# Performance work log

Hardware: AMD Instinct MI355X
Metric: run time of the kernel (lower is better)

Reference implementation:

```python
import jax, jax.numpy as jnp
import numpy as np

M0, M1, H = 128, 64, 8            # scalar mul, vector mul, num heads
AH0, AH1 = 16, 8                  # per-head irreps: 16x0e + 8x1e
D = M0 + 3 * M1                   # 320 node feature dim
DTP0 = M0 + M1                    # 192 scalar channels out of depthwise TP
DTP1 = M0 + 2 * M1                # 256 vector channels out of depthwise TP
WNUM = 2 * M0 + 3 * M1            # 448 TP path weights (uvu, edge mul=1)
RAD_IN, RAD_HID = 32, 64
N_NODES, N_EDGES = 10000, 160000
INV_SQRT3 = 1.0 / np.sqrt(3.0)    # CG norm for 1e x 1e -> 0e
INV_SQRT2 = 1.0 / np.sqrt(2.0)    # CG norm for 1e x 1e -> 1e


def _split(x, m0, m1):
    # e3nn layout: [m0 scalars | m1 vectors * 3 components]
    return x[..., :m0], x[..., m0:].reshape(x.shape[:-1] + (m1, 3))


def _silu(x):
    return x * jax.nn.sigmoid(x)


def _smooth_leaky(x, a=0.2):
    # SmoothLeakyReLU from equiformer
    return 0.5 * (1 + a) * x + 0.5 * (1 - a) * x * (2.0 * jax.nn.sigmoid(x) - 1.0)


def _dtp(s, v, e0, e1, w):
    # depthwise (uvu) tensor product of (M0x0e + M1x1e) with edge attr (1x0e + 1x1e)
    # s [E,M0], v [E,M1,3], e0 [E,1], e1 [E,3], w [E,WNUM] or [WNUM] (internal)
    w1, w2, w3, w4, w5 = jnp.split(w, [M0, 2 * M0, 2 * M0 + M1, 2 * M0 + 2 * M1], axis=-1)
    os1 = w1 * s * e0                                                  # 0e x 0e -> 0e
    os2 = w4 * (jnp.einsum('emc,ec->em', v, e1) * INV_SQRT3)           # 1e x 1e -> 0e
    ov1 = (w2 * s)[..., None] * e1[:, None, :]                         # 0e x 1e -> 1e
    ov2 = w3[..., None] * v * e0[..., None]                            # 1e x 0e -> 1e
    ov3 = w5[..., None] * (jnp.cross(v, e1[:, None, :]) * INV_SQRT2)   # 1e x 1e -> 1e
    return jnp.concatenate([os1, os2], -1), jnp.concatenate([ov1, ov2, ov3], -2)


def _forward(node_input, edge_src, edge_dst, edge_attr, edge_scalars,
             Wsrc_s, Wsrc_v, bsrc, Wdst_s, Wdst_v,
             rad_W1, rad_b1, rad_W2, rad_off,
             Wact_s, bact, Wact_v, Walpha, balpha, w_int,
             Wval_s, bval, Wval_v, alpha_dot, Wproj_s, bproj, Wproj_v):
    N = node_input.shape[0]
    E = edge_src.shape[0]
    s, v = _split(node_input, M0, M1)
    # merge_src / merge_dst: per-irrep linear (bias only on scalars of src)
    ms_s = s @ Wsrc_s + bsrc
    ms_v = jnp.einsum('nmc,mk->nkc', v, Wsrc_v)
    md_s = s @ Wdst_s
    md_v = jnp.einsum('nmc,mk->nkc', v, Wdst_v)
    msg_s = ms_s[edge_src] + md_s[edge_dst]          # [E, M0]
    msg_v = ms_v[edge_src] + md_v[edge_dst]          # [E, M1, 3]
    e0, e1 = edge_attr[:, :1], edge_attr[:, 1:4]
    # radial profile MLP -> edge-dependent TP weights
    w = _silu(edge_scalars @ rad_W1 + rad_b1) @ rad_W2 + rad_off       # [E, WNUM]
    ds, dv = _dtp(msg_s, msg_v, e0, e1, w)           # [E, DTP0], [E, DTP1, 3]
    # alpha branch: linear on TP scalars -> heads -> smooth leaky -> dot
    al = _smooth_leaky((ds @ Walpha + balpha).reshape(E, H, AH0))
    logits = jnp.einsum('ehk,hk->eh', al, alpha_dot[0])                # [E, H]
    # value branch: sep_act.lin + gate
    scal = ds @ Wact_s + bact                        # [E, M0+M1] scalars+gates
    gated_v = jnp.einsum('emc,mk->ekc', dv, Wact_v)  # [E, M1, 3]
    val_s = _silu(scal[:, :M0])
    val_v = gated_v * jax.nn.sigmoid(scal[:, M0:])[..., None]
    # sep_value: depthwise TP with internal weights + linear
    vs, vv = _dtp(val_s, val_v, e0, e1, w_int)
    out_s = vs @ Wval_s + bval                       # [E, H*AH0]
    out_v = jnp.einsum('emc,mk->ekc', vv, Wval_v)    # [E, H*AH1, 3]
    value = jnp.concatenate([out_s.reshape(E, H, AH0),
                             out_v.reshape(E, H, AH1 * 3)], axis=2)    # [E, H, 40]
    # softmax over incoming edges per destination node
    mx = jax.lax.stop_gradient(jax.ops.segment_max(logits, edge_dst, num_segments=N))
    mx = jnp.where(jnp.isfinite(mx), mx, 0.0)
    ex = jnp.exp(logits - mx[edge_dst])
    den = jax.ops.segment_sum(ex, edge_dst, num_segments=N)
    alpha = ex / (den[edge_dst] + 1e-16)             # [E, H]
    agg = jax.ops.segment_sum(value * alpha[..., None], edge_dst, num_segments=N)
    # heads2vec + output projection
    node_s = agg[:, :, :AH0].reshape(N, H * AH0)
    node_v = agg[:, :, AH0:].reshape(N, H * AH1, 3)
    po_s = node_s @ Wproj_s + bproj
    po_v = jnp.einsum('nmc,mk->nkc', node_v, Wproj_v)
    return jnp.concatenate([po_s, po_v.reshape(N, M1 * 3)], axis=1)


def _lin(key, fi, fo):
    return jax.random.normal(key, (fi, fo), jnp.float32) / np.sqrt(fi)


def setup_inputs() -> dict:
    ks = iter(jax.random.split(jax.random.key(0), 40))
    inp = {}
    inp['node_input'] = jax.random.normal(next(ks), (N_NODES, D), jnp.float32)
    inp['edge_src'] = jax.random.randint(next(ks), (N_EDGES,), 0, N_NODES)
    inp['edge_dst'] = jax.random.randint(next(ks), (N_EDGES,), 0, N_NODES)
    inp['edge_attr'] = jax.random.normal(next(ks), (N_EDGES, 4), jnp.float32)
    inp['edge_scalars'] = jax.random.normal(next(ks), (N_EDGES, RAD_IN), jnp.float32)
    inp['Wsrc_s'] = _lin(next(ks), M0, M0)
    inp['Wsrc_v'] = _lin(next(ks), M1, M1)
    inp['bsrc'] = 0.1 * jax.random.normal(next(ks), (M0,), jnp.float32)
    inp['Wdst_s'] = _lin(next(ks), M0, M0)
    inp['Wdst_v'] = _lin(next(ks), M1, M1)
    inp['rad_W1'] = _lin(next(ks), RAD_IN, RAD_HID)
    inp['rad_b1'] = 0.1 * jax.random.normal(next(ks), (RAD_HID,), jnp.float32)
    inp['rad_W2'] = _lin(next(ks), RAD_HID, WNUM)
    inp['rad_off'] = 0.1 * jax.random.normal(next(ks), (WNUM,), jnp.float32)
    inp['Wact_s'] = _lin(next(ks), DTP0, M0 + M1)
    inp['bact'] = 0.1 * jax.random.normal(next(ks), (M0 + M1,), jnp.float32)
    inp['Wact_v'] = _lin(next(ks), DTP1, M1)
    inp['Walpha'] = _lin(next(ks), DTP0, H * AH0)
    inp['balpha'] = 0.1 * jax.random.normal(next(ks), (H * AH0,), jnp.float32)
    inp['w_int'] = jax.random.normal(next(ks), (WNUM,), jnp.float32)
    inp['Wval_s'] = _lin(next(ks), DTP0, H * AH0)
    inp['bval'] = 0.1 * jax.random.normal(next(ks), (H * AH0,), jnp.float32)
    inp['Wval_v'] = _lin(next(ks), DTP1, H * AH1)
    inp['alpha_dot'] = jax.random.normal(next(ks), (1, H, AH0), jnp.float32) / np.sqrt(AH0)
    inp['Wproj_s'] = _lin(next(ks), H * AH0, M0)
    inp['bproj'] = 0.1 * jax.random.normal(next(ks), (M0,), jnp.float32)
    inp['Wproj_v'] = _lin(next(ks), H * AH1, M1)
    return inp


def reference(node_input, edge_src, edge_dst, edge_attr, edge_scalars,
              Wsrc_s, Wsrc_v, bsrc, Wdst_s, Wdst_v,
              rad_W1, rad_b1, rad_W2, rad_off,
              Wact_s, bact, Wact_v, Walpha, balpha, w_int,
              Wval_s, bval, Wval_v, alpha_dot, Wproj_s, bproj, Wproj_v):
    return _forward(node_input, edge_src, edge_dst, edge_attr, edge_scalars,
                    Wsrc_s, Wsrc_v, bsrc, Wdst_s, Wdst_v,
                    rad_W1, rad_b1, rad_W2, rad_off,
                    Wact_s, bact, Wact_v, Walpha, balpha, w_int,
                    Wval_s, bval, Wval_v, alpha_dot, Wproj_s, bproj, Wproj_v)
```

## Files before the change

kernel.cpp:

```cpp
#include <hip/hip_runtime.h>

#define NN 10000
#define NE 160000
#define INV_SQRT3f 0.57735026918962576f
#define INV_SQRT2f 0.70710678118654752f
#define VPL 640000

typedef short bshort8 __attribute__((ext_vector_type(8)));
typedef float floatx4 __attribute__((ext_vector_type(4)));
#define MFMA16(a,b,c) __builtin_amdgcn_mfma_f32_16x16x32_bf16((a),(b),(c),0,0,0)

__device__ __forceinline__ float sigm(float x){ return 1.f/(1.f+__expf(-x)); }
__device__ __forceinline__ float siluf(float x){ return x*sigm(x); }
__device__ __forceinline__ float sleaky(float x){ return 0.6f*x + 0.4f*x*(2.f*sigm(x)-1.f); }
__device__ __forceinline__ unsigned short f2bf(float f){
  return (unsigned short)((__float_as_uint(f) + 0x8000u)>>16);
}
__device__ __forceinline__ float bf2f(unsigned short h){
  return __uint_as_float(((unsigned)h)<<16);
}

#define O_W1   0
#define O_W2   2048
#define O_WAS  30720
#define O_WAVT 67584
#define O_WAVB 75776
#define O_WVS  83968
#define O_WVVT 108544
#define O_WVVB 116736
#define O_WALP 124928
#define SWZ_TOTAL 149504

__global__ __launch_bounds__(256) void k_init(float* __restrict__ num,
                                              float* __restrict__ den,
                                              int* __restrict__ cnt) {
  int i = blockIdx.x*256 + threadIdx.x;
  if (i < NN*320) num[i] = 0.f;
  if (i < NN*8) den[i] = 0.f;
  if (i < NN) cnt[i] = 0;
}

__global__ __launch_bounds__(256) void k_hist(const int* __restrict__ edst,
                                              int* __restrict__ cnt) {
  int e = blockIdx.x*256 + threadIdx.x;
  if (e < NE) atomicAdd(&cnt[edst[e]], 1);
}

__global__ __launch_bounds__(256) void k_scan(const int* __restrict__ cnt,
                                              int* __restrict__ offs) {
  __shared__ int wsum[4];
  const int tid = threadIdx.x;
  const int lane = tid & 63, wave = tid >> 6;
  int v[40]; int s = 0;
  #pragma unroll
  for (int j=0;j<40;j++){ int i = tid*40+j; v[j] = (i<NN)?cnt[i]:0; s += v[j]; }
  int incl = s;
  #pragma unroll
  for (int d=1; d<64; d<<=1) { int t = __shfl_up(incl, d, 64); if (lane>=d) incl += t; }
  if (lane==63) wsum[wave] = incl;
  __syncthreads();
  int wbase = 0;
  for (int w=0; w<wave; ++w) wbase += wsum[w];
  int excl = wbase + incl - s;
  #pragma unroll
  for (int j=0;j<40;j++){ int i = tid*40+j; if (i<NN) offs[i] = excl; excl += v[j]; }
}

__global__ __launch_bounds__(256) void k_scatter(const int* __restrict__ edst,
                                                 int* __restrict__ offs,
                                                 int* __restrict__ perm) {
  int e = blockIdx.x*256 + threadIdx.x;
  if (e < NE) {
    int pos = atomicAdd(&offs[edst[e]], 1);
    perm[pos] = e;
  }
}

__global__ __launch_bounds__(256) void node_pre(
    const float* __restrict__ x,
    const float* __restrict__ Wsrc_s, const float* __restrict__ Wsrc_v,
    const float* __restrict__ bsrc,
    const float* __restrict__ Wdst_s, const float* __restrict__ Wdst_v,
    float* __restrict__ ms_s, float* __restrict__ md_s,
    float* __restrict__ ms_v, float* __restrict__ md_v) {
  __shared__ __align__(16) float s_s[128*8];
  __shared__ __align__(16) float s_v[192*8];
  const int tid = threadIdx.x;
  const int n0 = blockIdx.x*8;
  for (int idx = tid; idx < 8*320; idx += 256) {
    int n = idx/320, d = idx - n*320;
    float val = x[(n0+n)*320 + d];
    if (d < 128) s_s[d*8+n] = val;
    else         s_v[(d-128)*8+n] = val;
  }
  __syncthreads();
  {
    int g = tid>>7, j = tid&127;
    float accs[4], accd[4];
    float b = bsrc[j];
    #pragma unroll
    for (int i=0;i<4;i++){ accs[i]=b; accd[i]=0.f; }
    for (int k=0;k<128;k++) {
      float w1 = Wsrc_s[k*128+j], w2 = Wdst_s[k*128+j];
      float4 sv = *(const float4*)&s_s[k*8+g*4];
      accs[0]+=sv.x*w1; accs[1]+=sv.y*w1; accs[2]+=sv.z*w1; accs[3]+=sv.w*w1;
      accd[0]+=sv.x*w2; accd[1]+=sv.y*w2; accd[2]+=sv.z*w2; accd[3]+=sv.w*w2;
    }
    #pragma unroll
    for (int i=0;i<4;i++){ int n=n0+g*4+i; ms_s[n*128+j]=accs[i]; md_s[n*128+j]=accd[i]; }
  }
  if (tid < 192) {
    int c = tid>>6, k = tid&63;
    float accs[8], accd[8];
    #pragma unroll
    for (int e=0;e<8;e++){ accs[e]=0.f; accd[e]=0.f; }
    for (int m=0;m<64;m++) {
      float w1 = Wsrc_v[m*64+k], w2 = Wdst_v[m*64+k];
      float4 v0 = *(const float4*)&s_v[(m*3+c)*8];
      float4 v1 = *(const float4*)&s_v[(m*3+c)*8+4];
      accs[0]+=v0.x*w1; accs[1]+=v0.y*w1; accs[2]+=v0.z*w1; accs[3]+=v0.w*w1;
      accs[4]+=v1.x*w1; accs[5]+=v1.y*w1; accs[6]+=v1.z*w1; accs[7]+=v1.w*w1;
      accd[0]+=v0.x*w2; accd[1]+=v0.y*w2; accd[2]+=v0.z*w2; accd[3]+=v0.w*w2;
      accd[4]+=v1.x*w2; accd[5]+=v1.y*w2; accd[6]+=v1.z*w2; accd[7]+=v1.w*w2;
    }
    #pragma unroll
    for (int e=0;e<8;e++){
      int n=n0+e;
      ms_v[c*VPL + n*64 + k] = accs[e];
      md_v[c*VPL + n*64 + k] = accd[e];
    }
  }
}

__global__ __launch_bounds__(256) void k_prep(
    const float* __restrict__ W1, const float* __restrict__ W2,
    const float* __restrict__ WAs, const float* __restrict__ WAv,
    const float* __restrict__ WVs, const float* __restrict__ WVv,
    const float* __restrict__ WAl,
    unsigned short* __restrict__ swz) {
  int s = blockIdx.x*256 + threadIdx.x;
  if (s >= SWZ_TOTAL) return;
  const float* src; int base, N, KT, rowOff;
  if      (s < 2048)  { base=O_W1;   src=W1;  N=64;  KT=1; rowOff=0; }
  else if (s < 30720) { base=O_W2;   src=W2;  N=448; KT=2; rowOff=0; }
  else if (s < 67584) { base=O_WAS;  src=WAs; N=192; KT=6; rowOff=0; }
  else if (s < 75776) { base=O_WAVT; src=WAv; N=64;  KT=4; rowOff=0; }
  else if (s < 83968) { base=O_WAVB; src=WAv; N=64;  KT=4; rowOff=128; }
  else if (s < 108544){ base=O_WVS;  src=WVs; N=128; KT=6; rowOff=0; }
  else if (s < 116736){ base=O_WVVT; src=WVv; N=64;  KT=4; rowOff=0; }
  else if (s < 124928){ base=O_WVVB; src=WVv; N=64;  KT=4; rowOff=128; }
  else                { base=O_WALP; src=WAl; N=128; KT=6; rowOff=0; }
  int loc = s - base;
  int j = loc & 7, l = (loc>>3)&63, kt = (loc>>9)%KT, nt = loc/(512*KT);
  int row = kt*32 + (l>>4)*8 + j + rowOff;
  int col = nt*16 + (l&15);
  swz[s] = f2bf(src[row*N + col]);
}

__global__ __launch_bounds__(256, 4) void e_all(
    const float* __restrict__ ms_s, const float* __restrict__ md_s,
    const float* __restrict__ ms_v, const float* __restrict__ md_v,
    const int* __restrict__ esrc, const int* __restrict__ edst,
    const int* __restrict__ perm,
    const float* __restrict__ eattr, const float* __restrict__ escal,
    const float* __restrict__ rad_b1, const float* __restrict__ rad_off,
    const float* __restrict__ bact, const float* __restrict__ w_int,
    const float* __restrict__ bval,
    const float* __restrict__ balpha, const float* __restrict__ alpha_dot,
    const unsigned short* __restrict__ swz,
    float* __restrict__ den, float* __restrict__ num) {
  __shared__ __align__(16) char smem[39040];
  unsigned short* sw   = (unsigned short*)smem;
  float* vout          = (float*)smem;
  unsigned short* ads  = (unsigned short*)(smem+14336);
  unsigned short* at1  = (unsigned short*)(smem+20736);
  unsigned short* advb = (unsigned short*)(smem+25088);
  unsigned short* aes  = (unsigned short*)(smem+25088);
  unsigned short* ah   = (unsigned short*)(smem+26368);
  float* s_e0 = (float*)(smem+38144);
  float* s_e1 = (float*)(smem+38208);
  float* s_ex = (float*)(smem+38400);
  int* s_src  = (int*)(smem+38912);
  int* s_dst  = (int*)(smem+38976);
  int* s_eid  = (int*)(smem+38848);
  const int tid  = threadIdx.x;
  const int lane = tid & 63, wave = tid >> 6;
  const int quad = lane >> 4, l15 = lane & 15;
  const int eb = blockIdx.x*16;

  if (tid < 16) {
    int eid = perm[eb+tid];
    s_eid[tid] = eid; s_src[tid] = esrc[eid]; s_dst[tid] = edst[eid];
  }
  __syncthreads();
  if (tid >= 64 && tid < 128) {
    int t = tid-64, e = t>>2, q = t&3;
    float a = eattr[s_eid[e]*4+q];
    if (q == 0) s_e0[e] = a; else s_e1[(q-1)*16+e] = a;
  }
  #pragma unroll
  for (int it = 0; it < 2; ++it) {
    int idx = tid + it*256;
    int e = idx>>5, i = idx&31;
    aes[e*40+i] = f2bf(escal[s_eid[e]*32+i]);
  }
  __syncthreads();

  {
    int nt = wave, col = nt*16 + l15;
    bshort8 a = *(const bshort8*)&aes[l15*40 + quad*8];
    bshort8 b = *(const bshort8*)&swz[O_W1 + (nt*64 + lane)*8];
    float bb = rad_b1[col];
    floatx4 acc = {bb,bb,bb,bb};
    acc = MFMA16(a, b, acc);
    #pragma unroll
    for (int r=0;r<4;r++) ah[(quad*4+r)*72 + col] = f2bf(siluf(acc[r]));
  }
  __syncthreads();

  {
    bshort8 ha0 = *(const bshort8*)&ah[l15*72 + quad*8];
    bshort8 ha1 = *(const bshort8*)&ah[l15*72 + 32 + quad*8];
    #pragma unroll
    for (int t=0;t<7;t++) {
      int nt = wave*7 + t, col = nt*16 + l15;
      float o = rad_off[col];
      floatx4 acc = {o,o,o,o};
      acc = MFMA16(ha0, *(const bshort8*)&swz[O_W2 + ((nt*2+0)*64+lane)*8], acc);
      acc = MFMA16(ha1, *(const bshort8*)&swz[O_W2 + ((nt*2+1)*64+lane)*8], acc);
      #pragma unroll
      for (int r=0;r<4;r++) sw[(quad*4+r)*448 + col] = f2bf(acc[r]);
    }
  }
  __syncthreads();

  #pragma unroll
  for (int it = 0; it < 8; ++it) {
    int t = tid + it*256;
    int m = t&127, e = t>>7;
    float msgs = ms_s[s_src[e]*128+m] + md_s[s_dst[e]*128+m];
    ads[e*200+m] = f2bf(bf2f(sw[e*448+m])*msgs*s_e0[e]);
    at1[e*136+m] = f2bf(bf2f(sw[e*448+128+m])*msgs);
  }
  #pragma unroll
  for (int it = 0; it < 4; ++it) {
    int t = tid + it*256;
    int k = t&63, e = t>>6;
    int sb = s_src[e]*64 + k, db = s_dst[e]*64 + k;
    float vx = ms_v[0*VPL+sb] + md_v[0*VPL+db];
    float vy = ms_v[1*VPL+sb] + md_v[1*VPL+db];
    float vz = ms_v[2*VPL+sb] + md_v[2*VPL+db];
    float ex1 = s_e1[0+e], ey1 = s_e1[16+e], ez1 = s_e1[32+e];
    float d = vx*ex1 + vy*ey1 + vz*ez1;
    ads[e*200+128+k] = f2bf(bf2f(sw[e*448+320+k])*d*INV_SQRT3f);
    float w3v = bf2f(sw[e*448+256+k])*s_e0[e];
    float w5  = bf2f(sw[e*448+384+k])*INV_SQRT2f;
    advb[0*2176 + e*136 + k] = f2bf(w3v*vx);
    advb[1*2176 + e*136 + k] = f2bf(w3v*vy);
    advb[2*2176 + e*136 + k] = f2bf(w3v*vz);
    advb[0*2176 + e*136 + 64+k] = f2bf(w5*(vy*ez1 - vz*ey1));
    advb[1*2176 + e*136 + 64+k] = f2bf(w5*(vz*ex1 - vx*ez1));
    advb[2*2176 + e*136 + 64+k] = f2bf(w5*(vx*ey1 - vy*ex1));
  }
  __syncthreads();

  floatx4 sc0, sc1, sc2, gsa, gb0, gb1, gb2;
  {
    bshort8 fa[6];
    #pragma unroll
    for (int kt=0;kt<6;kt++) fa[kt] = *(const bshort8*)&ads[l15*200 + kt*32 + quad*8];
    #pragma unroll
    for (int t=0;t<2;t++) {
      int h = wave*2 + t;
      int col = h*16 + l15;
      float bb = balpha[col];
      floatx4 acc = {bb,bb,bb,bb};
      #pragma unroll
      for (int kt=0;kt<6;kt++)
        acc = MFMA16(fa[kt], *(const bshort8*)&swz[O_WALP + ((h*6+kt)*64+lane)*8], acc);
      float ad = alpha_dot[col];
      #pragma unroll
      for (int r=0;r<4;r++) {
        float p = sleaky(acc[r])*ad;
        p += __shfl_xor(p, 1);
        p += __shfl_xor(p, 2);
        p += __shfl_xor(p, 4);
        p += __shfl_xor(p, 8);
        if (l15 == 0) {
          int row = quad*4 + r;
          float ex = __expf(p);
          s_ex[row*8+h] = ex;
          atomicAdd(&den[s_dst[row]*8+h], ex);
        }
      }
    }
    {
      float bb = bact[wave*16 + l15];
      floatx4 a0 = {bb,bb,bb,bb};
      #pragma unroll
      for (int kt=0;kt<6;kt++)
        a0 = MFMA16(fa[kt], *(const bshort8*)&swz[O_WAS + ((wave*6+kt)*64+lane)*8], a0);
      sc0 = a0;
    }
    {
      float bb = bact[(wave+4)*16 + l15];
      floatx4 a1 = {bb,bb,bb,bb};
      #pragma unroll
      for (int kt=0;kt<6;kt++)
        a1 = MFMA16(fa[kt], *(const bshort8*)&swz[O_WAS + (((wave+4)*6+kt)*64+lane)*8], a1);
      sc1 = a1;
    }
    {
      float bb = bact[(wave+8)*16 + l15];
      floatx4 a2 = {bb,bb,bb,bb};
      #pragma unroll
      for (int kt=0;kt<6;kt++)
        a2 = MFMA16(fa[kt], *(const bshort8*)&swz[O_WAS + (((wave+8)*6+kt)*64+lane)*8], a2);
      sc2 = a2;
    }
    bshort8 ft[4];
    #pragma unroll
    for (int kt=0;kt<4;kt++) ft[kt] = *(const bshort8*)&at1[l15*136 + kt*32 + quad*8];
    {
      floatx4 acc = {0.f,0.f,0.f,0.f};
      #pragma unroll
      for (int kt=0;kt<4;kt++)
        acc = MFMA16(ft[kt], *(const bshort8*)&swz[O_WAVT + ((wave*4+kt)*64+lane)*8], acc);
      gsa = acc;
    }
    #pragma unroll
    for (int c=0;c<3;c++) {
      floatx4 acc = {0.f,0.f,0.f,0.f};
      #pragma unroll
      for (int kt=0;kt<4;kt++) {
        bshort8 fb = *(const bshort8*)&advb[c*2176 + l15*136 + kt*32 + quad*8];
        acc = MFMA16(fb, *(const bshort8*)&swz[O_WAVB + ((wave*4+kt)*64+lane)*8], acc);
      }
      if (c==0) gb0 = acc; else if (c==1) gb1 = acc; else gb2 = acc;
    }
  }
  __syncthreads();

  {
    const int k = wave*16 + l15;
    #pragma unroll
    for (int r=0;r<4;r++) {
      int row = quad*4 + r;
      float e0 = s_e0[row];
      {
        float v = siluf(sc0[r]);
        ads[row*200+k] = f2bf(w_int[k]*v*e0);
        at1[row*136+k] = f2bf(w_int[128+k]*v);
      }
      {
        int m = 64+k;
        float v = siluf(sc1[r]);
        ads[row*200+m] = f2bf(w_int[m]*v*e0);
        at1[row*136+m] = f2bf(w_int[128+m]*v);
      }
      {
        float sg = sigm(sc2[r]);
        float gs = gsa[r];
        float ex1 = s_e1[0+row], ey1 = s_e1[16+row], ez1 = s_e1[32+row];
        float v0 = (gs*ex1 + gb0[r])*sg;
        float v1 = (gs*ey1 + gb1[r])*sg;
        float v2 = (gs*ez1 + gb2[r])*sg;
        float d = v0*ex1 + v1*ey1 + v2*ez1;
        ads[row*200+128+k] = f2bf(w_int[320+k]*d*INV_SQRT3f);
        float w3v = w_int[256+k]*e0;
        float w5  = w_int[384+k]*INV_SQRT2f;
        advb[0*2176 + row*136 + k] = f2bf(w3v*v0);
        advb[1*2176 + row*136 + k] = f2bf(w3v*v1);
        advb[2*2176 + row*136 + k] = f2bf(w3v*v2);
        advb[0*2176 + row*136 + 64+k] = f2bf(w5*(v1*ez1 - v2*ey1));
        advb[1*2176 + row*136 + 64+k] = f2bf(w5*(v2*ex1 - v0*ez1));
        advb[2*2176 + row*136 + 64+k] = f2bf(w5*(v0*ey1 - v1*ex1));
      }
    }
  }
  __syncthreads();

  {
    bshort8 fa[6];
    #pragma unroll
    for (int kt=0;kt<6;kt++) fa[kt] = *(const bshort8*)&ads[l15*200 + kt*32 + quad*8];
    #pragma unroll
    for (int t=0;t<2;t++) {
      int h = wave + 4*t;
      float bb = bval[h*16 + l15];
      floatx4 acc = {bb,bb,bb,bb};
      #pragma unroll
      for (int kt=0;kt<6;kt++)
        acc = MFMA16(fa[kt], *(const bshort8*)&swz[O_WVS + ((h*6+kt)*64+lane)*8], acc);
      #pragma unroll
      for (int r=0;r<4;r++) {
        int row = quad*4 + r;
        vout[row*128 + h*16 + l15] = acc[r]*s_ex[row*8+h];
      }
    }
  }
  __syncthreads();

  {
    int j = tid & 127, g = tid >> 7;
    int h = j>>4, jj = j&15;
    float acc = 0.f; int cur = s_dst[g*8];
    #pragma unroll
    for (int e = g*8; e < g*8+8; ++e) {
      int d = s_dst[e];
      if (d != cur) { atomicAdd(&num[cur*320 + h*40 + jj], acc); acc = 0.f; cur = d; }
      acc += vout[e*128 + j];
    }
    atomicAdd(&num[cur*320 + h*40 + jj], acc);
  }
  __syncthreads();

  {
    bshort8 ft[4];
    #pragma unroll
    for (int kt=0;kt<4;kt++) ft[kt] = *(const bshort8*)&at1[l15*136 + kt*32 + quad*8];
    floatx4 vsh = {0.f,0.f,0.f,0.f};
    #pragma unroll
    for (int kt=0;kt<4;kt++)
      vsh = MFMA16(ft[kt], *(const bshort8*)&swz[O_WVVT + ((wave*4+kt)*64+lane)*8], vsh);
    int k = wave*16 + l15;
    int h = k>>3, q = k&7;
    #pragma unroll
    for (int c=0;c<3;c++) {
      floatx4 acc = {0.f,0.f,0.f,0.f};
      #pragma unroll
      for (int kt=0;kt<4;kt++) {
        bshort8 fb = *(const bshort8*)&advb[c*2176 + l15*136 + kt*32 + quad*8];
        acc = MFMA16(fb, *(const bshort8*)&swz[O_WVVB + ((wave*4+kt)*64+lane)*8], acc);
      }
      #pragma unroll
      for (int r=0;r<4;r++) {
        int row = quad*4 + r;
        vout[row*192 + h*24 + q*3 + c] =
            (acc[r] + s_e1[c*16+row]*vsh[r]) * s_ex[row*8+h];
      }
    }
  }
  __syncthreads();

  #pragma unroll
  for (int it = 0; it < 2; ++it) {
    int idx = tid + it*256;
    if (idx < 384) {
      int g = idx/192, jj = idx - g*192;
      int h = jj/24, rr = jj - h*24;
      float acc = 0.f; int cur = s_dst[g*8];
      #pragma unroll
      for (int e = g*8; e < g*8+8; ++e) {
        int d = s_dst[e];
        if (d != cur) { atomicAdd(&num[cur*320 + h*40 + 16 + rr], acc); acc = 0.f; cur = d; }
        acc += vout[e*192 + jj];
      }
      atomicAdd(&num[cur*320 + h*40 + 16 + rr], acc);
    }
  }
}

__global__ __launch_bounds__(256) void node_post(
    const float* __restrict__ num, const float* __restrict__ den,
    const float* __restrict__ Wproj_s, const float* __restrict__ bproj,
    const float* __restrict__ Wproj_v, float* __restrict__ out) {
  __shared__ __align__(16) float s_ns[128*8];
  __shared__ __align__(16) float s_nv[192*8];
  const int tid = threadIdx.x;
  const int n0 = blockIdx.x*8;
  for (int idx = tid; idx < 8*320; idx += 256) {
    int n = idx/320, j = idx - n*320;
    int h = j/40, r = j - h*40;
    float a = num[(n0+n)*320+j] / (den[(n0+n)*8+h] + 1e-16f);
    if (r < 16) s_ns[(h*16+r)*8+n] = a;
    else        s_nv[(h*24 + (r-16))*8+n] = a;
  }
  __syncthreads();
  {
    int g = tid>>7, j = tid&127;
    float acc[4]; float b = bproj[j];
    #pragma unroll
    for (int i=0;i<4;i++) acc[i]=b;
    for (int k=0;k<128;k++) {
      float wv = Wproj_s[k*128+j];
      float4 s4 = *(const float4*)&s_ns[k*8+g*4];
      acc[0]+=s4.x*wv; acc[1]+=s4.y*wv; acc[2]+=s4.z*wv; acc[3]+=s4.w*wv;
    }
    #pragma unroll
    for (int i=0;i<4;i++) out[(n0+g*4+i)*320 + j] = acc[i];
  }
  if (tid < 192) {
    int c = tid>>6, k = tid&63;
    float acc[8];
    #pragma unroll
    for (int e=0;e<8;e++) acc[e]=0.f;
    for (int m=0;m<64;m++) {
      float wv = Wproj_v[m*64+k];
      float4 v0 = *(const float4*)&s_nv[(m*3+c)*8];
      float4 v1 = *(const float4*)&s_nv[(m*3+c)*8+4];
      acc[0]+=v0.x*wv; acc[1]+=v0.y*wv; acc[2]+=v0.z*wv; acc[3]+=v0.w*wv;
      acc[4]+=v1.x*wv; acc[5]+=v1.y*wv; acc[6]+=v1.z*wv; acc[7]+=v1.w*wv;
    }
    #pragma unroll
    for (int e=0;e<8;e++) out[(n0+e)*320 + 128 + k*3 + c] = acc[e];
  }
}

extern "C" void kernel_launch(void* const* d_in, const int* in_sizes, int n_in,
                              void* d_out, int out_size, void* d_ws, size_t ws_size,
                              hipStream_t stream) {
  (void)in_sizes; (void)n_in; (void)out_size; (void)ws_size;
  const float* node_input = (const float*)d_in[0];
  const int*   esrc       = (const int*)d_in[1];
  const int*   edst       = (const int*)d_in[2];
  const float* eattr      = (const float*)d_in[3];
  const float* escal      = (const float*)d_in[4];
  const float* Wsrc_s     = (const float*)d_in[5];
  const float* Wsrc_v     = (const float*)d_in[6];
  const float* bsrc       = (const float*)d_in[7];
  const float* Wdst_s     = (const float*)d_in[8];
  const float* Wdst_v     = (const float*)d_in[9];
  const float* rad_W1     = (const float*)d_in[10];
  const float* rad_b1     = (const float*)d_in[11];
  const float* rad_W2     = (const float*)d_in[12];
  const float* rad_off    = (const float*)d_in[13];
  const float* Wact_s     = (const float*)d_in[14];
  const float* bact       = (const float*)d_in[15];
  const float* Wact_v     = (const float*)d_in[16];
  const float* Walpha     = (const float*)d_in[17];
  const float* balpha     = (const float*)d_in[18];
  const float* w_int      = (const float*)d_in[19];
  const float* Wval_s     = (const float*)d_in[20];
  const float* bval       = (const float*)d_in[21];
  const float* Wval_v     = (const float*)d_in[22];
  const float* alpha_dot  = (const float*)d_in[23];
  const float* Wproj_s    = (const float*)d_in[24];
  const float* bproj      = (const float*)d_in[25];
  const float* Wproj_v    = (const float*)d_in[26];
  float* out = (float*)d_out;

  float* ws = (float*)d_ws;
  float* ms_s   = ws;
  float* md_s   = ws + 1280000;
  float* ms_v   = ws + 2560000;
  float* md_v   = ws + 4480000;
  float* den    = ws + 6400000;
  float* num    = ws + 6480000;
  unsigned short* swz = (unsigned short*)(ws + 9680000);
  int* cnt  = (int*)(ws + 9754752);
  int* offs = (int*)(ws + 9764752);
  int* perm = (int*)(ws + 9774752);

  k_prep<<<584, 256, 0, stream>>>(rad_W1, rad_W2, Wact_s, Wact_v, Wval_s, Wval_v, Walpha, swz);
  k_init<<<12500, 256, 0, stream>>>(num, den, cnt);
  k_hist<<<625, 256, 0, stream>>>(edst, cnt);
  k_scan<<<1, 256, 0, stream>>>(cnt, offs);
  k_scatter<<<625, 256, 0, stream>>>(edst, offs, perm);
  node_pre<<<1250, 256, 0, stream>>>(node_input, Wsrc_s, Wsrc_v, bsrc, Wdst_s, Wdst_v,
                                     ms_s, md_s, ms_v, md_v);
  e_all<<<10000, 256, 0, stream>>>(ms_s, md_s, ms_v, md_v, esrc, edst, perm, eattr, escal,
                                   rad_b1, rad_off, bact, w_int, bval,
                                   balpha, alpha_dot, swz, den, num);
  node_post<<<1250, 256, 0, stream>>>(num, den, Wproj_s, bproj, Wproj_v, out);
}
```

Before: 449.9 us.

## Keep radial scalar weights in registers and shrink shared memory for occupancy

The radial MLP output tiles for the scalar TP weights now stay in MFMA accumulators and are consumed directly, so only the vector-path weights (192 columns) go to shared memory. The scalar value-output reduction is done in registers with direct atomics instead of a shared-memory staging pass and barrier. The vector output staging is stored as bf16, and together these shrink LDS from about 39 KB to about 31 KB, with launch bounds raised to 5 blocks per CU. Storing the vector output in bf16 before accumulation adds rounding error, and register pressure rises under the tighter occupancy bound.

```diff
diff --git a/kernel.cpp b/kernel.cpp
--- a/kernel.cpp
+++ b/kernel.cpp
@@ -157,7 +157,7 @@
   swz[s] = f2bf(src[row*N + col]);
 }
 
-__global__ __launch_bounds__(256, 4) void e_all(
+__global__ __launch_bounds__(256, 5) void e_all(
     const float* __restrict__ ms_s, const float* __restrict__ md_s,
     const float* __restrict__ ms_v, const float* __restrict__ md_v,
     const int* __restrict__ esrc, const int* __restrict__ edst,
@@ -169,20 +169,20 @@
     const float* __restrict__ balpha, const float* __restrict__ alpha_dot,
     const unsigned short* __restrict__ swz,
     float* __restrict__ den, float* __restrict__ num) {
-  __shared__ __align__(16) char smem[39040];
-  unsigned short* sw   = (unsigned short*)smem;
-  float* vout          = (float*)smem;
-  unsigned short* ads  = (unsigned short*)(smem+14336);
-  unsigned short* at1  = (unsigned short*)(smem+20736);
-  unsigned short* advb = (unsigned short*)(smem+25088);
-  unsigned short* aes  = (unsigned short*)(smem+25088);
-  unsigned short* ah   = (unsigned short*)(smem+26368);
-  float* s_e0 = (float*)(smem+38144);
-  float* s_e1 = (float*)(smem+38208);
-  float* s_ex = (float*)(smem+38400);
-  int* s_src  = (int*)(smem+38912);
-  int* s_dst  = (int*)(smem+38976);
-  int* s_eid  = (int*)(smem+38848);
+  __shared__ __align__(16) char smem[30912];
+  unsigned short* swv   = (unsigned short*)smem;
+  unsigned short* voutv = (unsigned short*)smem;
+  unsigned short* ads  = (unsigned short*)(smem+6144);
+  unsigned short* at1  = (unsigned short*)(smem+12544);
+  unsigned short* advb = (unsigned short*)(smem+16896);
+  unsigned short* aes  = (unsigned short*)(smem+16896);
+  unsigned short* ah   = (unsigned short*)(smem+18176);
+  float* s_e0 = (float*)(smem+29952);
+  float* s_e1 = (float*)(smem+30016);
+  float* s_ex = (float*)(smem+30208);
+  int* s_eid  = (int*)(smem+30720);
+  int* s_src  = (int*)(smem+30784);
+  int* s_dst  = (int*)(smem+30848);
   const int tid  = threadIdx.x;
   const int lane = tid & 63, wave = tid >> 6;
   const int quad = lane >> 4, l15 = lane & 15;
@@ -218,30 +218,50 @@
   }
   __syncthreads();
 
+  floatx4 wA0, wA1, wB0, wB1;
   {
     bshort8 ha0 = *(const bshort8*)&ah[l15*72 + quad*8];
     bshort8 ha1 = *(const bshort8*)&ah[l15*72 + 32 + quad*8];
-    #pragma unroll
-    for (int t=0;t<7;t++) {
-      int nt = wave*7 + t, col = nt*16 + l15;
-      float o = rad_off[col];
+    { int nt = wave;       float o = rad_off[nt*16+l15]; floatx4 a = {o,o,o,o};
+      a = MFMA16(ha0, *(const bshort8*)&swz[O_W2 + ((nt*2+0)*64+lane)*8], a);
+      a = MFMA16(ha1, *(const bshort8*)&swz[O_W2 + ((nt*2+1)*64+lane)*8], a); wA0 = a; }
+    { int nt = 8+wave;     float o = rad_off[nt*16+l15]; floatx4 a = {o,o,o,o};
+      a = MFMA16(ha0, *(const bshort8*)&swz[O_W2 + ((nt*2+0)*64+lane)*8], a);
+      a = MFMA16(ha1, *(const bshort8*)&swz[O_W2 + ((nt*2+1)*64+lane)*8], a); wA1 = a; }
+    { int nt = 4+wave;     float o = rad_off[nt*16+l15]; floatx4 a = {o,o,o,o};
+      a = MFMA16(ha0, *(const bshort8*)&swz[O_W2 + ((nt*2+0)*64+lane)*8], a);
+      a = MFMA16(ha1, *(const bshort8*)&swz[O_W2 + ((nt*2+1)*64+lane)*8], a); wB0 = a; }
+    { int nt = 12+wave;    float o = rad_off[nt*16+l15]; floatx4 a = {o,o,o,o};
+      a = MFMA16(ha0, *(const bshort8*)&swz[O_W2 + ((nt*2+0)*64+lane)*8], a);
+      a = MFMA16(ha1, *(const bshort8*)&swz[O_W2 + ((nt*2+1)*64+lane)*8], a); wB1 = a; }
+    #pragma unroll
+    for (int t=0;t<3;t++) {
+      int nt = 16 + wave*3 + t;
+      float o = rad_off[nt*16+l15];
       floatx4 acc = {o,o,o,o};
       acc = MFMA16(ha0, *(const bshort8*)&swz[O_W2 + ((nt*2+0)*64+lane)*8], acc);
       acc = MFMA16(ha1, *(const bshort8*)&swz[O_W2 + ((nt*2+1)*64+lane)*8], acc);
       #pragma unroll
-      for (int r=0;r<4;r++) sw[(quad*4+r)*448 + col] = f2bf(acc[r]);
-    }
-  }
-  __syncthreads();
-
-  #pragma unroll
-  for (int it = 0; it < 8; ++it) {
-    int t = tid + it*256;
-    int m = t&127, e = t>>7;
-    float msgs = ms_s[s_src[e]*128+m] + md_s[s_dst[e]*128+m];
-    ads[e*200+m] = f2bf(bf2f(sw[e*448+m])*msgs*s_e0[e]);
-    at1[e*136+m] = f2bf(bf2f(sw[e*448+128+m])*msgs);
-  }
+      for (int r=0;r<4;r++) swv[(quad*4+r)*192 + (nt-16)*16 + l15] = f2bf(acc[r]);
+    }
+  }
+  {
+    const int mA = wave*16 + l15, mB = 64 + wave*16 + l15;
+    #pragma unroll
+    for (int r=0;r<4;r++) {
+      int e = quad*4 + r;
+      float e0 = s_e0[e];
+      int sb = s_src[e]*128, db = s_dst[e]*128;
+      float msA = ms_s[sb+mA] + md_s[db+mA];
+      ads[e*200+mA] = f2bf(wA0[r]*msA*e0);
+      at1[e*136+mA] = f2bf(wA1[r]*msA);
+      float msB = ms_s[sb+mB] + md_s[db+mB];
+      ads[e*200+mB] = f2bf(wB0[r]*msB*e0);
+      at1[e*136+mB] = f2bf(wB1[r]*msB);
+    }
+  }
+  __syncthreads();
+
   #pragma unroll
   for (int it = 0; it < 4; ++it) {
     int t = tid + it*256;
@@ -252,9 +272,9 @@
     float vz = ms_v[2*VPL+sb] + md_v[2*VPL+db];
     float ex1 = s_e1[0+e], ey1 = s_e1[16+e], ez1 = s_e1[32+e];
     float d = vx*ex1 + vy*ey1 + vz*ez1;
-    ads[e*200+128+k] = f2bf(bf2f(sw[e*448+320+k])*d*INV_SQRT3f);
-    float w3v = bf2f(sw[e*448+256+k])*s_e0[e];
-    float w5  = bf2f(sw[e*448+384+k])*INV_SQRT2f;
+    ads[e*200+128+k] = f2bf(bf2f(swv[e*192 + 64+k])*d*INV_SQRT3f);
+    float w3v = bf2f(swv[e*192 + k])*s_e0[e];
+    float w5  = bf2f(swv[e*192 + 128+k])*INV_SQRT2f;
     advb[0*2176 + e*136 + k] = f2bf(w3v*vx);
     advb[1*2176 + e*136 + k] = f2bf(w3v*vy);
     advb[2*2176 + e*136 + k] = f2bf(w3v*vz);
@@ -392,28 +412,17 @@
       #pragma unroll
       for (int kt=0;kt<6;kt++)
         acc = MFMA16(fa[kt], *(const bshort8*)&swz[O_WVS + ((h*6+kt)*64+lane)*8], acc);
+      float vac = 0.f; int cur = s_dst[quad*4];
       #pragma unroll
       for (int r=0;r<4;r++) {
         int row = quad*4 + r;
-        vout[row*128 + h*16 + l15] = acc[r]*s_ex[row*8+h];
-      }
-    }
-  }
-  __syncthreads();
-
-  {
-    int j = tid & 127, g = tid >> 7;
-    int h = j>>4, jj = j&15;
-    float acc = 0.f; int cur = s_dst[g*8];
-    #pragma unroll
-    for (int e = g*8; e < g*8+8; ++e) {
-      int d = s_dst[e];
-      if (d != cur) { atomicAdd(&num[cur*320 + h*40 + jj], acc); acc = 0.f; cur = d; }
-      acc += vout[e*128 + j];
-    }
-    atomicAdd(&num[cur*320 + h*40 + jj], acc);
-  }
-  __syncthreads();
+        int d = s_dst[row];
+        if (d != cur) { atomicAdd(&num[cur*320 + h*40 + l15], vac); vac = 0.f; cur = d; }
+        vac += acc[r]*s_ex[row*8+h];
+      }
+      atomicAdd(&num[cur*320 + h*40 + l15], vac);
+    }
+  }
 
   {
     bshort8 ft[4];
@@ -436,8 +445,8 @@
       #pragma unroll
       for (int r=0;r<4;r++) {
         int row = quad*4 + r;
-        vout[row*192 + h*24 + q*3 + c] =
-            (acc[r] + s_e1[c*16+row]*vsh[r]) * s_ex[row*8+h];
+        voutv[row*192 + h*24 + q*3 + c] =
+            f2bf((acc[r] + s_e1[c*16+row]*vsh[r]) * s_ex[row*8+h]);
       }
     }
   }
@@ -454,7 +463,7 @@
       for (int e = g*8; e < g*8+8; ++e) {
         int d = s_dst[e];
         if (d != cur) { atomicAdd(&num[cur*320 + h*40 + 16 + rr], acc); acc = 0.f; cur = d; }
-        acc += vout[e*192 + jj];
+        acc += bf2f(voutv[e*192 + jj]);
       }
       atomicAdd(&num[cur*320 + h*40 + 16 + rr], acc);
     }
```

New measurement: 464.8 us. 1.03x slower.
